# Kernel tuning notes

Measured on AMD Instinct MI355X. Metric: run time of the kernel, lower is better.

Reference implementation:

```python
import jax, jax.numpy as jnp
import numpy as np

N_USER, N_ITEM, N_REL = 200000, 100000, 64
DIM = 64
S_UU = S_UI = S_IU = S_II = 8
BATCH = 65536
MAX_RATING = 5.0


def setup_inputs() -> dict:
    key = jax.random.key(0)
    ks = jax.random.split(key, 24)
    inp = {}
    # query batch
    inp['u'] = jax.random.randint(ks[0], (BATCH,), 0, N_USER)
    inp['v'] = jax.random.randint(ks[1], (BATCH,), 0, N_ITEM)
    # embedding tables (init std=0.8 as in the torch code)
    inp['usr_feat'] = 0.8 * jax.random.normal(ks[2], (N_USER, DIM), jnp.float32)
    inp['item_feat'] = 0.8 * jax.random.normal(ks[3], (N_ITEM, DIM), jnp.float32)
    inp['rel_feat'] = 0.8 * jax.random.normal(ks[4], (N_REL, DIM), jnp.float32)
    # precomputed sampled neighbor tables (built once in __init__ in the original)
    inp['neigh_uu'] = jax.random.randint(ks[5], (N_USER, S_UU), 0, N_USER)
    inp['neigh_uu_st'] = jax.random.uniform(ks[6], (N_USER, S_UU), jnp.float32)
    inp['neigh_ui'] = jax.random.randint(ks[7], (N_USER, S_UI), 0, N_ITEM)
    inp['neigh_ui_rat'] = MAX_RATING * jax.random.uniform(ks[8], (N_USER, S_UI), jnp.float32)
    inp['neigh_ui_vot'] = jax.random.uniform(ks[9], (N_USER, S_UI), jnp.float32)
    inp['neigh_ui_tim'] = jax.random.uniform(ks[10], (N_USER, S_UI), jnp.float32)
    inp['neigh_iu'] = jax.random.randint(ks[11], (N_ITEM, S_IU), 0, N_USER)
    inp['neigh_iu_rat'] = MAX_RATING * jax.random.uniform(ks[12], (N_ITEM, S_IU), jnp.float32)
    inp['neigh_iu_vot'] = jax.random.uniform(ks[13], (N_ITEM, S_IU), jnp.float32)
    inp['neigh_iu_tim'] = jax.random.uniform(ks[14], (N_ITEM, S_IU), jnp.float32)
    inp['neigh_ii'] = jax.random.randint(ks[15], (N_ITEM, S_II), 0, N_ITEM)
    inp['neigh_ir'] = jax.random.randint(ks[16], (N_ITEM, S_II), 0, N_REL)
    # aggregator transforms (one per side)
    sc = 1.0 / np.sqrt(DIM)
    inp['Wu'] = sc * jax.random.normal(ks[17], (DIM, DIM), jnp.float32)
    inp['bu'] = jnp.zeros((DIM,), jnp.float32)
    inp['Wv'] = sc * jax.random.normal(ks[18], (DIM, DIM), jnp.float32)
    inp['bv'] = jnp.zeros((DIM,), jnp.float32)
    return inp


def reference(u, v, usr_feat, item_feat, rel_feat,
              neigh_uu, neigh_uu_st, neigh_ui, neigh_ui_rat, neigh_ui_vot, neigh_ui_tim,
              neigh_iu, neigh_iu_rat, neigh_iu_vot, neigh_iu_tim, neigh_ii, neigh_ir,
              Wu, bu, Wv, bv):
    u_emb = usr_feat[u]                                   # [B, D]
    v_emb = item_feat[v]                                  # [B, D]

    # ---- user-side aggregation ----
    # social neighbors, weighted by softmax over social tie strength
    uu_nei = usr_feat[neigh_uu[u]]                        # [B, S, D]
    w_uu = jax.nn.softmax(neigh_uu_st[u], axis=-1)        # [B, S]
    agg_uu = jnp.einsum('bs,bsd->bd', w_uu, uu_nei)
    # interacted items, weighted by rating * vote * time recency
    ui_nei = item_feat[neigh_ui[u]]                       # [B, S, D]
    s_ui = neigh_ui_rat[u] * neigh_ui_vot[u] * neigh_ui_tim[u]
    w_ui = jax.nn.softmax(s_ui, axis=-1)
    agg_ui = jnp.einsum('bs,bsd->bd', w_ui, ui_nei)
    user_h = jax.nn.relu((u_emb + agg_uu + agg_ui) @ Wu + bu)

    # ---- item-side aggregation ----
    # users who interacted with the item, weighted like above
    iu_nei = usr_feat[neigh_iu[v]]                        # [B, S, D]
    s_iu = neigh_iu_rat[v] * neigh_iu_vot[v] * neigh_iu_tim[v]
    w_iu = jax.nn.softmax(s_iu, axis=-1)
    agg_iu = jnp.einsum('bs,bsd->bd', w_iu, iu_nei)
    # KG neighbors with user-relation attention (KGCN-style)
    ii_nei = item_feat[neigh_ii[v]]                       # [B, S, D]
    rel = rel_feat[neigh_ir[v]]                           # [B, S, D]
    att = jnp.einsum('bd,bsd->bs', u_emb, rel)            # user-relation score
    w_ii = jax.nn.softmax(att, axis=-1)
    agg_ii = jnp.einsum('bs,bsd->bd', w_ii, ii_nei)
    item_h = jax.nn.relu((v_emb + agg_iu + agg_ii) @ Wv + bv)

    # rating prediction
    score = jax.nn.sigmoid(jnp.sum(user_h * item_h, axis=-1)) * MAX_RATING
    return score
```

## Files before the change

kernel.cpp:

```cpp
#include <hip/hip_runtime.h>
#include <math.h>

constexpr int DIM = 64;
constexpr int S = 8;
constexpr int WPB = 4;
constexpr int BLOCK = WPB * 64;
constexpr int GRID = 1024;

typedef __attribute__((ext_vector_type(8))) __bf16 bf16x8;
typedef __attribute__((ext_vector_type(4))) float  f32x4;

#define LDS_FENCE() asm volatile("s_waitcnt lgkmcnt(0)" ::: "memory")
#define SCHED_PIN() __builtin_amdgcn_sched_barrier(0)

template <int CTRL>
__device__ __forceinline__ float dppx(float x) {
    return __builtin_bit_cast(float,
        __builtin_amdgcn_mov_dpp(__builtin_bit_cast(int, x), CTRL, 0xf, 0xf, true));
}
#define XOR1 0xB1
#define XOR2 0x4E

__device__ __forceinline__ unsigned pk_bf16(float a, float b) {
    unsigned ua = __builtin_bit_cast(unsigned, a);
    unsigned ub = __builtin_bit_cast(unsigned, b);
    ua = (ua + 0x8000u) >> 16;
    ub = (ub + 0x8000u) & 0xffff0000u;
    return ua | ub;
}

__device__ __forceinline__ void octet_softmax(float sc, float* wout) {
    float m = sc;
    m = fmaxf(m, dppx<XOR1>(m));
    m = fmaxf(m, dppx<XOR2>(m));
    m = fmaxf(m, __shfl_xor(m, 4));
    float e = __expf(sc - m);
    float s = e;
    s += dppx<XOR1>(s);
    s += dppx<XOR2>(s);
    s += __shfl_xor(s, 4);
    float w = e / s;
    #pragma unroll
    for (int k = 0; k < 8; k++) wout[k] = __shfl(w, k);
}

__device__ __forceinline__ void matvec_h(
    float xv, int lane, unsigned short* xw,
    const bf16x8* xa00, const bf16x8* xa01,
    const bf16x8* xa10, const bf16x8* xa11,
    const unsigned* bf,
    float b0, float b1, float b2, float b3,
    float& h0, float& h1, float& h2, float& h3)
{
    LDS_FENCE();
    const unsigned xb = __builtin_bit_cast(unsigned, xv);
    const unsigned hb = (xb + 0x8000u) & 0xffff0000u;
    const float xl = xv - __builtin_bit_cast(float, hb);
    xw[lane]      = (unsigned short)(hb >> 16);
    xw[64 + lane] = (unsigned short)((__builtin_bit_cast(unsigned, xl) + 0x8000u) >> 16);
    LDS_FENCE();

    f32x4 a0 = {0.f, 0.f, 0.f, 0.f};
    f32x4 a1 = a0, a2 = a0, a3 = a0;

    {
        const bf16x8 ah = *xa00, al = *xa01;
        const bf16x8 w0 = *(const bf16x8*)(bf);
        const bf16x8 w1 = *(const bf16x8*)(bf + 256);
        const bf16x8 w2 = *(const bf16x8*)(bf + 512);
        const bf16x8 w3 = *(const bf16x8*)(bf + 768);
        a0 = __builtin_amdgcn_mfma_f32_16x16x32_bf16(ah, w0, a0, 0, 0, 0);
        a0 = __builtin_amdgcn_mfma_f32_16x16x32_bf16(al, w0, a0, 0, 0, 0);
        a1 = __builtin_amdgcn_mfma_f32_16x16x32_bf16(ah, w1, a1, 0, 0, 0);
        a1 = __builtin_amdgcn_mfma_f32_16x16x32_bf16(al, w1, a1, 0, 0, 0);
        a2 = __builtin_amdgcn_mfma_f32_16x16x32_bf16(ah, w2, a2, 0, 0, 0);
        a2 = __builtin_amdgcn_mfma_f32_16x16x32_bf16(al, w2, a2, 0, 0, 0);
        a3 = __builtin_amdgcn_mfma_f32_16x16x32_bf16(ah, w3, a3, 0, 0, 0);
        a3 = __builtin_amdgcn_mfma_f32_16x16x32_bf16(al, w3, a3, 0, 0, 0);
    }
    {
        const bf16x8 ah = *xa10, al = *xa11;
        const bf16x8 w0 = *(const bf16x8*)(bf + 1024);
        const bf16x8 w1 = *(const bf16x8*)(bf + 1280);
        const bf16x8 w2 = *(const bf16x8*)(bf + 1536);
        const bf16x8 w3 = *(const bf16x8*)(bf + 1792);
        a0 = __builtin_amdgcn_mfma_f32_16x16x32_bf16(ah, w0, a0, 0, 0, 0);
        a0 = __builtin_amdgcn_mfma_f32_16x16x32_bf16(al, w0, a0, 0, 0, 0);
        a1 = __builtin_amdgcn_mfma_f32_16x16x32_bf16(ah, w1, a1, 0, 0, 0);
        a1 = __builtin_amdgcn_mfma_f32_16x16x32_bf16(al, w1, a1, 0, 0, 0);
        a2 = __builtin_amdgcn_mfma_f32_16x16x32_bf16(ah, w2, a2, 0, 0, 0);
        a2 = __builtin_amdgcn_mfma_f32_16x16x32_bf16(al, w2, a2, 0, 0, 0);
        a3 = __builtin_amdgcn_mfma_f32_16x16x32_bf16(ah, w3, a3, 0, 0, 0);
        a3 = __builtin_amdgcn_mfma_f32_16x16x32_bf16(al, w3, a3, 0, 0, 0);
    }

    h0 = fmaxf(a0[0] + b0, 0.f);
    h1 = fmaxf(a1[0] + b1, 0.f);
    h2 = fmaxf(a2[0] + b2, 0.f);
    h3 = fmaxf(a3[0] + b3, 0.f);
}

__global__ __launch_bounds__(BLOCK, 4)
void sestkgcn_kernel(
    const int*   __restrict__ u_idx,
    const int*   __restrict__ v_idx,
    const float* __restrict__ usr_feat,
    const float* __restrict__ item_feat,
    const float* __restrict__ rel_feat,
    const int*   __restrict__ neigh_uu,
    const float* __restrict__ neigh_uu_st,
    const int*   __restrict__ neigh_ui,
    const float* __restrict__ neigh_ui_rat,
    const float* __restrict__ neigh_ui_vot,
    const float* __restrict__ neigh_ui_tim,
    const int*   __restrict__ neigh_iu,
    const float* __restrict__ neigh_iu_rat,
    const float* __restrict__ neigh_iu_vot,
    const float* __restrict__ neigh_iu_tim,
    const int*   __restrict__ neigh_ii,
    const int*   __restrict__ neigh_ir,
    const float* __restrict__ Wu,
    const float* __restrict__ bu,
    const float* __restrict__ Wv,
    const float* __restrict__ bv,
    float*       __restrict__ out,
    int n)
{
    __shared__ unsigned sBFu[2048];
    __shared__ unsigned sBFv[2048];
    __shared__ __align__(16) unsigned short sX[WPB][128];

    const int tid = threadIdx.x;
    for (int i = tid; i < 2048; i += BLOCK) {
        const int d = i & 3, l = (i >> 2) & 63, f = i >> 8;
        const int row = ((f >> 2) << 5) + ((l >> 4) << 3) + (d << 1);
        const int col = ((f & 3) << 4) + (l & 15);
        sBFu[i] = pk_bf16(Wu[row * DIM + col], Wu[(row + 1) * DIM + col]);
        sBFv[i] = pk_bf16(Wv[row * DIM + col], Wv[(row + 1) * DIM + col]);
    }
    __syncthreads();

    const int wave = tid >> 6;
    const int lane = tid & 63;
    const int ls   = lane & 7;
    const int g    = lane >> 4;
    const int c    = lane & 15;

    unsigned short* xw = &sX[wave][0];
    const bf16x8* xa00 = (const bf16x8*)&sX[wave][g * 8];
    const bf16x8* xa01 = (const bf16x8*)&sX[wave][64 + g * 8];
    const bf16x8* xa10 = (const bf16x8*)&sX[wave][32 + g * 8];
    const bf16x8* xa11 = (const bf16x8*)&sX[wave][96 + g * 8];
    const unsigned* bfu = &sBFu[lane * 4];
    const unsigned* bfv = &sBFv[lane * 4];

    const float bu0 = bu[c], bu1 = bu[c + 16], bu2 = bu[c + 32], bu3 = bu[c + 48];
    const float bv0 = bv[c], bv1 = bv[c + 16], bv2 = bv[c + 32], bv3 = bv[c + 48];

    const int stride = GRID * WPB;
    int b = blockIdx.x * WPB + wave;
    if (b >= n) return;

    int u = u_idx[b], v = v_idx[b];
    int bc1 = b + stride; if (bc1 >= n) bc1 = b;
    int u1 = u_idx[bc1], v1 = v_idx[bc1];

    unsigned u8 = (unsigned)u << 3, v8 = (unsigned)v << 3;
    int4 iuu0 = ((const int4*)(neigh_uu + u8))[0];
    int4 iuu1 = ((const int4*)(neigh_uu + u8))[1];
    int4 iui0 = ((const int4*)(neigh_ui + u8))[0];
    int4 iui1 = ((const int4*)(neigh_ui + u8))[1];
    int4 iiu0 = ((const int4*)(neigh_iu + v8))[0];
    int4 iiu1 = ((const int4*)(neigh_iu + v8))[1];
    int4 iii0 = ((const int4*)(neigh_ii + v8))[0];
    int4 iii1 = ((const int4*)(neigh_ii + v8))[1];
    int4 iir0 = ((const int4*)(neigh_ir + v8))[0];
    int4 iir1 = ((const int4*)(neigh_ir + v8))[1];
    float suu_r = neigh_uu_st[u8 + ls];
    float uir = neigh_ui_rat[u8 + ls], uiv = neigh_ui_vot[u8 + ls], uit = neigh_ui_tim[u8 + ls];
    float iur = neigh_iu_rat[v8 + ls], ivv = neigh_iu_vot[v8 + ls], ivt = neigh_iu_tim[v8 + ls];
    float ud_c = usr_feat[((unsigned)u << 6) | (unsigned)lane];
    float vd_c = item_feat[((unsigned)v << 6) | (unsigned)lane];
    float ruu[S], rui[S], riu[S], rii[S];
    {
        const int nuu[S] = {iuu0.x, iuu0.y, iuu0.z, iuu0.w, iuu1.x, iuu1.y, iuu1.z, iuu1.w};
        const int nui[S] = {iui0.x, iui0.y, iui0.z, iui0.w, iui1.x, iui1.y, iui1.z, iui1.w};
        const int niu[S] = {iiu0.x, iiu0.y, iiu0.z, iiu0.w, iiu1.x, iiu1.y, iiu1.z, iiu1.w};
        const int nii[S] = {iii0.x, iii0.y, iii0.z, iii0.w, iii1.x, iii1.y, iii1.z, iii1.w};
        #pragma unroll
        for (int s = 0; s < S; s++) ruu[s] = usr_feat[((unsigned)nuu[s] << 6) | (unsigned)lane];
        #pragma unroll
        for (int s = 0; s < S; s++) rui[s] = item_feat[((unsigned)nui[s] << 6) | (unsigned)lane];
        #pragma unroll
        for (int s = 0; s < S; s++) riu[s] = usr_feat[((unsigned)niu[s] << 6) | (unsigned)lane];
        #pragma unroll
        for (int s = 0; s < S; s++) rii[s] = item_feat[((unsigned)nii[s] << 6) | (unsigned)lane];
    }
    float ud_n = 0.f, vd_n = 0.f;

    while (true) {
        float rr[S];
        {
            const int nir[S] = {iir0.x, iir0.y, iir0.z, iir0.w, iir1.x, iir1.y, iir1.z, iir1.w};
            #pragma unroll
            for (int s = 0; s < S; s++) rr[s] = rel_feat[((unsigned)nir[s] << 6) | (unsigned)lane];
        }
        const unsigned u81 = (unsigned)u1 << 3, v81 = (unsigned)v1 << 3;
        iuu0 = ((const int4*)(neigh_uu + u81))[0];
        iuu1 = ((const int4*)(neigh_uu + u81))[1];
        iui0 = ((const int4*)(neigh_ui + u81))[0];
        iui1 = ((const int4*)(neigh_ui + u81))[1];
        iiu0 = ((const int4*)(neigh_iu + v81))[0];
        iiu1 = ((const int4*)(neigh_iu + v81))[1];
        iii0 = ((const int4*)(neigh_ii + v81))[0];
        iii1 = ((const int4*)(neigh_ii + v81))[1];
        iir0 = ((const int4*)(neigh_ir + v81))[0];
        iir1 = ((const int4*)(neigh_ir + v81))[1];
        int b2c = b + 2 * stride; if (b2c >= n) b2c = b;
        const int u2 = u_idx[b2c], v2 = v_idx[b2c];
        SCHED_PIN();

        float w[S];
        octet_softmax(suu_r, w);
        float agg_uu = 0.f;
        #pragma unroll
        for (int s = 0; s < S; s++) agg_uu = fmaf(w[s], ruu[s], agg_uu);

        octet_softmax(uir * uiv * uit, w);
        float agg_ui = 0.f;
        #pragma unroll
        for (int s = 0; s < S; s++) agg_ui = fmaf(w[s], rui[s], agg_ui);

        float hu0, hu1, hu2, hu3;
        matvec_h(ud_c + agg_uu + agg_ui, lane, xw, xa00, xa01, xa10, xa11,
                 bfu, bu0, bu1, bu2, bu3, hu0, hu1, hu2, hu3);

        octet_softmax(iur * ivv * ivt, w);
        float agg_iu = 0.f;
        #pragma unroll
        for (int s = 0; s < S; s++) agg_iu = fmaf(w[s], riu[s], agg_iu);

        {
            float p[S];
            #pragma unroll
            for (int s = 0; s < S; s++) p[s] = ud_c * rr[s];

            float m1[4];
            #pragma unroll
            for (int i = 0; i < 4; i++) {
                float lo = (lane & 1) ? p[2 * i + 1] : p[2 * i];
                float hi = (lane & 1) ? p[2 * i]     : p[2 * i + 1];
                m1[i] = lo + dppx<XOR1>(hi);
            }
            float m2[2];
            #pragma unroll
            for (int i = 0; i < 2; i++) {
                float lo = (lane & 2) ? m1[2 * i + 1] : m1[2 * i];
                float hi = (lane & 2) ? m1[2 * i]     : m1[2 * i + 1];
                m2[i] = lo + dppx<XOR2>(hi);
            }
            float lo = (lane & 4) ? m2[1] : m2[0];
            float hi = (lane & 4) ? m2[0] : m2[1];
            float att = lo + __shfl_xor(hi, 4);
            att += __shfl_xor(att, 8);
            att += __shfl_xor(att, 16);
            att += __shfl_xor(att, 32);
            octet_softmax(att, w);
        }
        float agg_ii = 0.f;
        #pragma unroll
        for (int s = 0; s < S; s++) agg_ii = fmaf(w[s], rii[s], agg_ii);

        {
            const int nuu[S] = {iuu0.x, iuu0.y, iuu0.z, iuu0.w, iuu1.x, iuu1.y, iuu1.z, iuu1.w};
            const int nui[S] = {iui0.x, iui0.y, iui0.z, iui0.w, iui1.x, iui1.y, iui1.z, iui1.w};
            const int niu[S] = {iiu0.x, iiu0.y, iiu0.z, iiu0.w, iiu1.x, iiu1.y, iiu1.z, iiu1.w};
            const int nii[S] = {iii0.x, iii0.y, iii0.z, iii0.w, iii1.x, iii1.y, iii1.z, iii1.w};
            #pragma unroll
            for (int s = 0; s < S; s++) ruu[s] = usr_feat[((unsigned)nuu[s] << 6) | (unsigned)lane];
            #pragma unroll
            for (int s = 0; s < S; s++) rui[s] = item_feat[((unsigned)nui[s] << 6) | (unsigned)lane];
            #pragma unroll
            for (int s = 0; s < S; s++) riu[s] = usr_feat[((unsigned)niu[s] << 6) | (unsigned)lane];
            #pragma unroll
            for (int s = 0; s < S; s++) rii[s] = item_feat[((unsigned)nii[s] << 6) | (unsigned)lane];
        }
        suu_r = neigh_uu_st[u81 + ls];
        uir = neigh_ui_rat[u81 + ls]; uiv = neigh_ui_vot[u81 + ls]; uit = neigh_ui_tim[u81 + ls];
        iur = neigh_iu_rat[v81 + ls]; ivv = neigh_iu_vot[v81 + ls]; ivt = neigh_iu_tim[v81 + ls];
        ud_n = usr_feat[((unsigned)u1 << 6) | (unsigned)lane];
        vd_n = item_feat[((unsigned)v1 << 6) | (unsigned)lane];
        SCHED_PIN();

        float hv0, hv1, hv2, hv3;
        matvec_h(vd_c + agg_iu + agg_ii, lane, xw, xa00, xa01, xa10, xa11,
                 bfv, bv0, bv1, bv2, bv3, hv0, hv1, hv2, hv3);

        float p = hu0 * hv0 + hu1 * hv1 + hu2 * hv2 + hu3 * hv3;
        p += dppx<XOR1>(p);
        p += dppx<XOR2>(p);
        p += __shfl_xor(p, 4);
        p += __shfl_xor(p, 8);
        if (lane == 0) out[b] = 5.0f / (1.0f + __expf(-p));

        b += stride;
        if (b >= n) break;
        u = u1; v = v1; u1 = u2; v1 = v2;
        ud_c = ud_n; vd_c = vd_n;
    }
}

extern "C" void kernel_launch(void* const* d_in, const int* in_sizes, int n_in,
                              void* d_out, int out_size, void* d_ws, size_t ws_size,
                              hipStream_t stream) {
    const int*   u_idx        = (const int*)  d_in[0];
    const int*   v_idx        = (const int*)  d_in[1];
    const float* usr_feat     = (const float*)d_in[2];
    const float* item_feat    = (const float*)d_in[3];
    const float* rel_feat     = (const float*)d_in[4];
    const int*   neigh_uu     = (const int*)  d_in[5];
    const float* neigh_uu_st  = (const float*)d_in[6];
    const int*   neigh_ui     = (const int*)  d_in[7];
    const float* neigh_ui_rat = (const float*)d_in[8];
    const float* neigh_ui_vot = (const float*)d_in[9];
    const float* neigh_ui_tim = (const float*)d_in[10];
    const int*   neigh_iu     = (const int*)  d_in[11];
    const float* neigh_iu_rat = (const float*)d_in[12];
    const float* neigh_iu_vot = (const float*)d_in[13];
    const float* neigh_iu_tim = (const float*)d_in[14];
    const int*   neigh_ii     = (const int*)  d_in[15];
    const int*   neigh_ir     = (const int*)  d_in[16];
    const float* Wu           = (const float*)d_in[17];
    const float* bu           = (const float*)d_in[18];
    const float* Wv           = (const float*)d_in[19];
    const float* bv           = (const float*)d_in[20];
    float*       out          = (float*)d_out;

    const int n = in_sizes[0];
    int blocks = (n + WPB - 1) / WPB;
    if (blocks > GRID) blocks = GRID;
    sestkgcn_kernel<<<blocks, BLOCK, 0, stream>>>(
        u_idx, v_idx, usr_feat, item_feat, rel_feat,
        neigh_uu, neigh_uu_st, neigh_ui, neigh_ui_rat, neigh_ui_vot, neigh_ui_tim,
        neigh_iu, neigh_iu_rat, neigh_iu_vot, neigh_iu_tim, neigh_ii, neigh_ir,
        Wu, bu, Wv, bv, out, n);
}
```

Baseline: 253.6 us.

## Gather neighbor embeddings from fp16 table copies converted each call

Adds a pre-pass kernel that converts the user and item embedding tables to fp16 in workspace, then gathers neighbor rows from these half-size tables to cut random-gather bytes. It also doubles the grid cap and raises the launch-bounds occupancy hint. The conversion rewrites the full tables (about 77 MB read, 38 MB written) on every call, which may cost more than the gathers save for 65k queries, and it adds fp16 rounding error.

```diff
diff --git a/kernel.cpp b/kernel.cpp
--- a/kernel.cpp
+++ b/kernel.cpp
@@ -5,10 +5,18 @@
 constexpr int S = 8;
 constexpr int WPB = 4;
 constexpr int BLOCK = WPB * 64;
-constexpr int GRID = 1024;
+constexpr int GRID = 2048;
+
+constexpr int N_USER = 200000;
+constexpr int N_ITEM = 100000;
+constexpr size_t USR16_BYTES  = (size_t)N_USER * DIM * 2;
+constexpr size_t ITEM16_BYTES = (size_t)N_ITEM * DIM * 2;
+constexpr size_t WS_NEEDED    = USR16_BYTES + ITEM16_BYTES;
 
 typedef __attribute__((ext_vector_type(8))) __bf16 bf16x8;
 typedef __attribute__((ext_vector_type(4))) float  f32x4;
+typedef __attribute__((ext_vector_type(8))) float     f32x8;
+typedef __attribute__((ext_vector_type(8))) _Float16  f16x8;
 
 #define LDS_FENCE() asm volatile("s_waitcnt lgkmcnt(0)" ::: "memory")
 #define SCHED_PIN() __builtin_amdgcn_sched_barrier(0)
@@ -100,7 +108,22 @@
     h3 = fmaxf(a3[0] + b3, 0.f);
 }
 
-__global__ __launch_bounds__(BLOCK, 4)
+__global__ __launch_bounds__(256)
+void cvt16_kernel(const float* __restrict__ usr_feat, const float* __restrict__ item_feat,
+                  _Float16* __restrict__ usr16, _Float16* __restrict__ item16,
+                  int n8u, int n8t)
+{
+    const int i = blockIdx.x * 256 + threadIdx.x;
+    if (i >= n8t) return;
+    const float* src = (i < n8u) ? usr_feat : item_feat;
+    _Float16*   dst = (i < n8u) ? usr16    : item16;
+    const int j = (i < n8u) ? i : (i - n8u);
+    const f32x8 v = ((const f32x8*)src)[j];
+    ((f16x8*)dst)[j] = __builtin_convertvector(v, f16x8);
+}
+
+template <bool USE16>
+__global__ __launch_bounds__(BLOCK, 8)
 void sestkgcn_kernel(
     const int*   __restrict__ u_idx,
     const int*   __restrict__ v_idx,
@@ -123,6 +146,8 @@
     const float* __restrict__ bu,
     const float* __restrict__ Wv,
     const float* __restrict__ bv,
+    const _Float16* __restrict__ usr16,
+    const _Float16* __restrict__ item16,
     float*       __restrict__ out,
     int n)
 {
@@ -188,13 +213,25 @@
         const int niu[S] = {iiu0.x, iiu0.y, iiu0.z, iiu0.w, iiu1.x, iiu1.y, iiu1.z, iiu1.w};
         const int nii[S] = {iii0.x, iii0.y, iii0.z, iii0.w, iii1.x, iii1.y, iii1.z, iii1.w};
         #pragma unroll
-        for (int s = 0; s < S; s++) ruu[s] = usr_feat[((unsigned)nuu[s] << 6) | (unsigned)lane];
-        #pragma unroll
-        for (int s = 0; s < S; s++) rui[s] = item_feat[((unsigned)nui[s] << 6) | (unsigned)lane];
-        #pragma unroll
-        for (int s = 0; s < S; s++) riu[s] = usr_feat[((unsigned)niu[s] << 6) | (unsigned)lane];
-        #pragma unroll
-        for (int s = 0; s < S; s++) rii[s] = item_feat[((unsigned)nii[s] << 6) | (unsigned)lane];
+        for (int s = 0; s < S; s++) {
+            const unsigned ix = ((unsigned)nuu[s] << 6) | (unsigned)lane;
+            ruu[s] = USE16 ? (float)usr16[ix] : usr_feat[ix];
+        }
+        #pragma unroll
+        for (int s = 0; s < S; s++) {
+            const unsigned ix = ((unsigned)nui[s] << 6) | (unsigned)lane;
+            rui[s] = USE16 ? (float)item16[ix] : item_feat[ix];
+        }
+        #pragma unroll
+        for (int s = 0; s < S; s++) {
+            const unsigned ix = ((unsigned)niu[s] << 6) | (unsigned)lane;
+            riu[s] = USE16 ? (float)usr16[ix] : usr_feat[ix];
+        }
+        #pragma unroll
+        for (int s = 0; s < S; s++) {
+            const unsigned ix = ((unsigned)nii[s] << 6) | (unsigned)lane;
+            rii[s] = USE16 ? (float)item16[ix] : item_feat[ix];
+        }
     }
     float ud_n = 0.f, vd_n = 0.f;
 
@@ -277,13 +314,25 @@
             const int niu[S] = {iiu0.x, iiu0.y, iiu0.z, iiu0.w, iiu1.x, iiu1.y, iiu1.z, iiu1.w};
             const int nii[S] = {iii0.x, iii0.y, iii0.z, iii0.w, iii1.x, iii1.y, iii1.z, iii1.w};
             #pragma unroll
-            for (int s = 0; s < S; s++) ruu[s] = usr_feat[((unsigned)nuu[s] << 6) | (unsigned)lane];
-            #pragma unroll
-            for (int s = 0; s < S; s++) rui[s] = item_feat[((unsigned)nui[s] << 6) | (unsigned)lane];
-            #pragma unroll
-            for (int s = 0; s < S; s++) riu[s] = usr_feat[((unsigned)niu[s] << 6) | (unsigned)lane];
-            #pragma unroll
-            for (int s = 0; s < S; s++) rii[s] = item_feat[((unsigned)nii[s] << 6) | (unsigned)lane];
+            for (int s = 0; s < S; s++) {
+                const unsigned ix = ((unsigned)nuu[s] << 6) | (unsigned)lane;
+                ruu[s] = USE16 ? (float)usr16[ix] : usr_feat[ix];
+            }
+            #pragma unroll
+            for (int s = 0; s < S; s++) {
+                const unsigned ix = ((unsigned)nui[s] << 6) | (unsigned)lane;
+                rui[s] = USE16 ? (float)item16[ix] : item_feat[ix];
+            }
+            #pragma unroll
+            for (int s = 0; s < S; s++) {
+                const unsigned ix = ((unsigned)niu[s] << 6) | (unsigned)lane;
+                riu[s] = USE16 ? (float)usr16[ix] : usr_feat[ix];
+            }
+            #pragma unroll
+            for (int s = 0; s < S; s++) {
+                const unsigned ix = ((unsigned)nii[s] << 6) | (unsigned)lane;
+                rii[s] = USE16 ? (float)item16[ix] : item_feat[ix];
+            }
         }
         suu_r = neigh_uu_st[u81 + ls];
         uir = neigh_ui_rat[u81 + ls]; uiv = neigh_ui_vot[u81 + ls]; uit = neigh_ui_tim[u81 + ls];
@@ -339,9 +388,25 @@
     const int n = in_sizes[0];
     int blocks = (n + WPB - 1) / WPB;
     if (blocks > GRID) blocks = GRID;
-    sestkgcn_kernel<<<blocks, BLOCK, 0, stream>>>(
-        u_idx, v_idx, usr_feat, item_feat, rel_feat,
-        neigh_uu, neigh_uu_st, neigh_ui, neigh_ui_rat, neigh_ui_vot, neigh_ui_tim,
-        neigh_iu, neigh_iu_rat, neigh_iu_vot, neigh_iu_tim, neigh_ii, neigh_ir,
-        Wu, bu, Wv, bv, out, n);
-}
+
+    const bool use16 = (d_ws != nullptr) && (ws_size >= WS_NEEDED);
+    if (use16) {
+        _Float16* usr16  = (_Float16*)d_ws;
+        _Float16* item16 = (_Float16*)((char*)d_ws + USR16_BYTES);
+        const int n8u = N_USER * DIM / 8;
+        const int n8t = n8u + N_ITEM * DIM / 8;
+        cvt16_kernel<<<(n8t + 255) / 256, 256, 0, stream>>>(
+            usr_feat, item_feat, usr16, item16, n8u, n8t);
+        sestkgcn_kernel<true><<<blocks, BLOCK, 0, stream>>>(
+            u_idx, v_idx, usr_feat, item_feat, rel_feat,
+            neigh_uu, neigh_uu_st, neigh_ui, neigh_ui_rat, neigh_ui_vot, neigh_ui_tim,
+            neigh_iu, neigh_iu_rat, neigh_iu_vot, neigh_iu_tim, neigh_ii, neigh_ir,
+            Wu, bu, Wv, bv, usr16, item16, out, n);
+    } else {
+        sestkgcn_kernel<false><<<blocks, BLOCK, 0, stream>>>(
+            u_idx, v_idx, usr_feat, item_feat, rel_feat,
+            neigh_uu, neigh_uu_st, neigh_ui, neigh_ui_rat, neigh_ui_vot, neigh_ui_tim,
+            neigh_iu, neigh_iu_rat, neigh_iu_vot, neigh_iu_tim, neigh_ii, neigh_ir,
+            Wu, bu, Wv, bv, nullptr, nullptr, out, n);
+    }
+}
```

After: 613.2 us. +141.8%, slower.
